# Kernel tuning notes

Measured on AMD Instinct MI355X. Metric: run time of the kernel, lower is better.

## Reference

```python
import jax, jax.numpy as jnp
import numpy as np

K = 16          # max neighbors per ball query
RADIUS = 1.0    # ball radius
SEQ_LEN = 4
N_POINTS = 8192


def ball_query_idx(xyz, radius, k):
    """PointNet++-style ball query of xyz against itself.
    xyz: [N, 3]. Returns [N, k] int32: the first k in-radius source indices
    (in ascending index order, matching the CUDA kernel's scan order),
    padded with the first in-radius index when fewer than k are found.
    Self-distance is 0 < radius so every row has at least one hit.
    """
    n = xyz.shape[0]
    # squared pairwise distances via the matmul expansion: ||a-b||^2 = ||a||^2 + ||b||^2 - 2 a.b
    sq = jnp.sum(xyz * xyz, axis=-1)                          # [N]
    d2 = sq[:, None] + sq[None, :] - 2.0 * (xyz @ xyz.T)      # [N, N]
    cand = jnp.where(d2 < radius * radius, jnp.arange(n, dtype=jnp.int32)[None, :], n)
    firstk = jnp.sort(cand, axis=-1)[:, :k]                   # first k hits in index order, n = no-hit sentinel
    first = firstk[:, :1]                                     # first in-radius index (always valid)
    return jnp.where(firstk == n, first, firstk)              # pad missing slots with first hit


def setup_inputs() -> dict:
    key = jax.random.key(0)
    k1, k2 = jax.random.split(key)
    pc_source = jax.random.normal(k1, (1, N_POINTS, 3), dtype=jnp.float32)
    pred_flow = jax.random.normal(k2, (SEQ_LEN, N_POINTS, 3), dtype=jnp.float32)
    return {"pc_source": pc_source, "pred_flow": pred_flow}


def reference(pc_source, pred_flow):
    # idx from pc_source (batch 1), broadcast across the sequence (idx.repeat in torch)
    idx = ball_query_idx(pc_source[0], RADIUS, K)             # [N, k]
    flow = jnp.transpose(pred_flow, (0, 2, 1))                # [S, 3, N]
    nn_flow = flow[:, :, idx]                                 # grouping_operation -> [S, 3, N, k]
    diff = flow[..., None] - nn_flow                          # [S, 3, N, k]
    # p=2 norm over the channel dim (safe sqrt: self-neighbor diff is exactly 0)
    dist = jnp.sqrt(jnp.maximum(jnp.sum(diff * diff, axis=1), 1e-24))  # [S, N, k]
    # .mean(dim=-1) over k, then .mean(dim=-1) over N (no weights branch), then .mean() over S
    return dist.mean(axis=-1).mean(axis=-1).mean()
```

## Files before the change

kernel.cpp:

```cpp
#include <hip/hip_runtime.h>
#include <math.h>

#define NP 8192
#define SEQ 4
#define KNN 16
#define R2 1.0f

__global__ __launch_bounds__(256, 8) void ballq_fused(
    const float* __restrict__ xyz,
    const float* __restrict__ pf,
    float* __restrict__ partial)
{
    const int lane = threadIdx.x & 63;
    const int wv   = threadIdx.x >> 6;
    const int i    = (blockIdx.x << 2) + wv;

    const float xi = xyz[3 * i + 0];
    const float yi = xyz[3 * i + 1];
    const float zi = xyz[3 * i + 2];

    int myNbr = -1;
    int cnt   = 0;
    int first = -1;

    for (int base = 0; base < NP; base += 256) {
        unsigned long long masks[4];
#pragma unroll
        for (int u = 0; u < 4; ++u) {
            const int j = base + (u << 6) + lane;
            const float dx = xyz[3 * j + 0] - xi;
            const float dy = xyz[3 * j + 1] - yi;
            const float dz = xyz[3 * j + 2] - zi;
            masks[u] = __ballot(dx * dx + dy * dy + dz * dz < R2);
        }
#pragma unroll
        for (int u = 0; u < 4; ++u) {
            unsigned long long m = masks[u];
            const int sub = base + (u << 6);
            while (m && cnt < KNN) {
                const int b = __builtin_ctzll(m);
                const int j = sub + b;
                if (cnt == 0) first = j;
                if (lane == cnt) myNbr = j;
                ++cnt;
                m &= m - 1;
            }
        }
        if (cnt >= KNN) break;
    }
    if (myNbr < 0) myNbr = first;

    const int k = lane & 15;
    const int s = lane >> 4;
    const int j = __shfl(myNbr, k);
    const size_t oi = ((size_t)s * NP + i) * 3;
    const size_t oj = ((size_t)s * NP + j) * 3;
    const float dx = pf[oi + 0] - pf[oj + 0];
    const float dy = pf[oi + 1] - pf[oj + 1];
    const float dz = pf[oi + 2] - pf[oj + 2];
    float d = sqrtf(fmaxf(dx * dx + dy * dy + dz * dz, 1e-24f));

#pragma unroll
    for (int off = 32; off > 0; off >>= 1) d += __shfl_xor(d, off);

    __shared__ float sacc[4];
    if (lane == 0) sacc[wv] = d;
    __syncthreads();
    if (threadIdx.x == 0)
        partial[blockIdx.x] = sacc[0] + sacc[1] + sacc[2] + sacc[3];
}

__global__ __launch_bounds__(256) void ballq_reduce(
    const float* __restrict__ partial, int n, float* __restrict__ out)
{
    float s = 0.0f;
    for (int i = threadIdx.x; i < n; i += 256) s += partial[i];
#pragma unroll
    for (int off = 32; off > 0; off >>= 1) s += __shfl_xor(s, off);
    __shared__ float w[4];
    const int lane = threadIdx.x & 63, wv = threadIdx.x >> 6;
    if (lane == 0) w[wv] = s;
    __syncthreads();
    if (threadIdx.x == 0)
        out[0] = (w[0] + w[1] + w[2] + w[3]) * (1.0f / (float)(SEQ * NP * KNN));
}

extern "C" void kernel_launch(void* const* d_in, const int* in_sizes, int n_in,
                              void* d_out, int out_size, void* d_ws, size_t ws_size,
                              hipStream_t stream) {
    const float* xyz = (const float*)d_in[0];
    const float* pf  = (const float*)d_in[1];
    float* partial   = (float*)d_ws;
    float* out       = (float*)d_out;

    const int nblocks = NP / 4;
    ballq_fused<<<nblocks, 256, 0, stream>>>(xyz, pf, partial);
    ballq_reduce<<<1, 256, 0, stream>>>(partial, nblocks, out);
}
```

Before: 73.49 us.

## Prefetch next candidate tile in registers and replace reduce kernel with atomics

The ball-query scan now software-pipelines its candidate loads: while the current 256-point tile is tested, the next tile's coordinates are loaded into registers, which hides global load latency in the early-exit loop. The separate reduction kernel is removed; each block atomically adds its scaled partial sum into the output, which is zeroed first with a memset. The occupancy hint in launch_bounds is also dropped. The extra registers may lower occupancy, and float atomics make the summation order nondeterministic.

```diff
diff --git a/kernel.cpp b/kernel.cpp
--- a/kernel.cpp
+++ b/kernel.cpp
@@ -5,11 +5,12 @@
 #define SEQ 4
 #define KNN 16
 #define R2 1.0f
+#define SCALE (1.0f / (float)(SEQ * NP * KNN))
 
-__global__ __launch_bounds__(256, 8) void ballq_fused(
+__global__ __launch_bounds__(256) void ballq_fused(
     const float* __restrict__ xyz,
     const float* __restrict__ pf,
-    float* __restrict__ partial)
+    float* __restrict__ out)
 {
     const int lane = threadIdx.x & 63;
     const int wv   = threadIdx.x >> 6;
@@ -23,16 +24,34 @@
     int cnt   = 0;
     int first = -1;
 
+    float cx[4], cy[4], cz[4];
+#pragma unroll
+    for (int u = 0; u < 4; ++u) {
+        const int j = (u << 6) + lane;
+        cx[u] = xyz[3 * j + 0];
+        cy[u] = xyz[3 * j + 1];
+        cz[u] = xyz[3 * j + 2];
+    }
+
     for (int base = 0; base < NP; base += 256) {
+        float nx[4], ny[4], nz[4];
+#pragma unroll
+        for (int u = 0; u < 4; ++u) {
+            const int j = (base + 256 + (u << 6) + lane) & (NP - 1);
+            nx[u] = xyz[3 * j + 0];
+            ny[u] = xyz[3 * j + 1];
+            nz[u] = xyz[3 * j + 2];
+        }
+
         unsigned long long masks[4];
 #pragma unroll
         for (int u = 0; u < 4; ++u) {
-            const int j = base + (u << 6) + lane;
-            const float dx = xyz[3 * j + 0] - xi;
-            const float dy = xyz[3 * j + 1] - yi;
-            const float dz = xyz[3 * j + 2] - zi;
+            const float dx = cx[u] - xi;
+            const float dy = cy[u] - yi;
+            const float dz = cz[u] - zi;
             masks[u] = __ballot(dx * dx + dy * dy + dz * dz < R2);
         }
+
 #pragma unroll
         for (int u = 0; u < 4; ++u) {
             unsigned long long m = masks[u];
@@ -47,6 +66,9 @@
             }
         }
         if (cnt >= KNN) break;
+
+#pragma unroll
+        for (int u = 0; u < 4; ++u) { cx[u] = nx[u]; cy[u] = ny[u]; cz[u] = nz[u]; }
     }
     if (myNbr < 0) myNbr = first;
 
@@ -67,22 +89,7 @@
     if (lane == 0) sacc[wv] = d;
     __syncthreads();
     if (threadIdx.x == 0)
-        partial[blockIdx.x] = sacc[0] + sacc[1] + sacc[2] + sacc[3];
-}
-
-__global__ __launch_bounds__(256) void ballq_reduce(
-    const float* __restrict__ partial, int n, float* __restrict__ out)
-{
-    float s = 0.0f;
-    for (int i = threadIdx.x; i < n; i += 256) s += partial[i];
-#pragma unroll
-    for (int off = 32; off > 0; off >>= 1) s += __shfl_xor(s, off);
-    __shared__ float w[4];
-    const int lane = threadIdx.x & 63, wv = threadIdx.x >> 6;
-    if (lane == 0) w[wv] = s;
-    __syncthreads();
-    if (threadIdx.x == 0)
-        out[0] = (w[0] + w[1] + w[2] + w[3]) * (1.0f / (float)(SEQ * NP * KNN));
+        atomicAdd(out, (sacc[0] + sacc[1] + sacc[2] + sacc[3]) * SCALE);
 }
 
 extern "C" void kernel_launch(void* const* d_in, const int* in_sizes, int n_in,
@@ -90,10 +97,8 @@
                               hipStream_t stream) {
     const float* xyz = (const float*)d_in[0];
     const float* pf  = (const float*)d_in[1];
-    float* partial   = (float*)d_ws;
     float* out       = (float*)d_out;
 
-    const int nblocks = NP / 4;
-    ballq_fused<<<nblocks, 256, 0, stream>>>(xyz, pf, partial);
-    ballq_reduce<<<1, 256, 0, stream>>>(partial, nblocks, out);
+    hipMemsetAsync(out, 0, sizeof(float), stream);
+    ballq_fused<<<NP / 4, 256, 0, stream>>>(xyz, pf, out);
 }
```

After: 88.64 us. 20.6% more time.

## Scan 1024 candidates per wave via per-lane bitmasks and prefix-sum compaction

Applied to the files above, without the earlier changes.

Each lane now loads 16 consecutive points with 12 float4 loads and builds a 16-bit in-radius mask, so one wave tests 1024 candidates per iteration instead of 256. Hits are ranked with a wave prefix sum and written in index order to a shared-memory slot array, replacing the serial ctz loop that ran over ballot masks. This cuts per-iteration overhead and widens loads, but uses many more registers (48 floats), drops the occupancy hint in launch bounds, and may scan more points than needed before the early exit.

```diff
diff --git a/kernel.cpp b/kernel.cpp
--- a/kernel.cpp
+++ b/kernel.cpp
@@ -5,8 +5,12 @@
 #define SEQ 4
 #define KNN 16
 #define R2 1.0f
+#define NBLK (NP / 4)
+#define WSZ 1024
+#define CPL 16
+#define SCALE (1.0f / (float)(SEQ * NP * KNN))
 
-__global__ __launch_bounds__(256, 8) void ballq_fused(
+__global__ __launch_bounds__(256) void ballq_main(
     const float* __restrict__ xyz,
     const float* __restrict__ pf,
     float* __restrict__ partial)
@@ -19,36 +23,55 @@
     const float yi = xyz[3 * i + 1];
     const float zi = xyz[3 * i + 2];
 
+    __shared__ int slots[4][KNN];
+
     int myNbr = -1;
     int cnt   = 0;
-    int first = -1;
 
-    for (int base = 0; base < NP; base += 256) {
-        unsigned long long masks[4];
+    for (int base = 0; base < NP; base += WSZ) {
+        float f[48];
+        const float4* p = (const float4*)xyz + ((3 * base) >> 2) + 12 * lane;
 #pragma unroll
-        for (int u = 0; u < 4; ++u) {
-            const int j = base + (u << 6) + lane;
-            const float dx = xyz[3 * j + 0] - xi;
-            const float dy = xyz[3 * j + 1] - yi;
-            const float dz = xyz[3 * j + 2] - zi;
-            masks[u] = __ballot(dx * dx + dy * dy + dz * dz < R2);
+        for (int j = 0; j < 12; ++j) ((float4*)f)[j] = p[j];
+
+        unsigned m = 0;
+#pragma unroll
+        for (int u = 0; u < CPL; ++u) {
+            const float dx = f[3 * u + 0] - xi;
+            const float dy = f[3 * u + 1] - yi;
+            const float dz = f[3 * u + 2] - zi;
+            m |= (unsigned)(dx * dx + dy * dy + dz * dz < R2) << u;
         }
+
+        const int c = __popc(m);
+        int pfx = c;
 #pragma unroll
-        for (int u = 0; u < 4; ++u) {
-            unsigned long long m = masks[u];
-            const int sub = base + (u << 6);
-            while (m && cnt < KNN) {
-                const int b = __builtin_ctzll(m);
-                const int j = sub + b;
-                if (cnt == 0) first = j;
-                if (lane == cnt) myNbr = j;
-                ++cnt;
-                m &= m - 1;
-            }
+        for (int off = 1; off < 64; off <<= 1) {
+            const int t = __shfl_up(pfx, off);
+            if (lane >= off) pfx += t;
         }
+        const int excl  = pfx - c;
+        const int total = __shfl(pfx, 63);
+
+        unsigned mm = m;
+        int r = 0;
+        while (mm) {
+            const int rank = cnt + excl + r;
+            if (rank >= KNN) break;
+            const int b = __builtin_ctz(mm);
+            slots[wv][rank] = base + CPL * lane + b;
+            mm &= mm - 1;
+            ++r;
+        }
+
+        const int newcnt = cnt + total;
+        if (lane >= cnt && lane < KNN && lane < newcnt)
+            myNbr = slots[wv][lane];
+        cnt = newcnt;
         if (cnt >= KNN) break;
     }
-    if (myNbr < 0) myNbr = first;
+    const int firstHit = __shfl(myNbr, 0);
+    if (myNbr < 0) myNbr = firstHit;
 
     const int k = lane & 15;
     const int s = lane >> 4;
@@ -71,10 +94,10 @@
 }
 
 __global__ __launch_bounds__(256) void ballq_reduce(
-    const float* __restrict__ partial, int n, float* __restrict__ out)
+    const float* __restrict__ partial, float* __restrict__ out)
 {
     float s = 0.0f;
-    for (int i = threadIdx.x; i < n; i += 256) s += partial[i];
+    for (int t = threadIdx.x; t < NBLK; t += 256) s += partial[t];
 #pragma unroll
     for (int off = 32; off > 0; off >>= 1) s += __shfl_xor(s, off);
     __shared__ float w[4];
@@ -82,7 +105,7 @@
     if (lane == 0) w[wv] = s;
     __syncthreads();
     if (threadIdx.x == 0)
-        out[0] = (w[0] + w[1] + w[2] + w[3]) * (1.0f / (float)(SEQ * NP * KNN));
+        out[0] = (w[0] + w[1] + w[2] + w[3]) * SCALE;
 }
 
 extern "C" void kernel_launch(void* const* d_in, const int* in_sizes, int n_in,
@@ -93,7 +116,6 @@
     float* partial   = (float*)d_ws;
     float* out       = (float*)d_out;
 
-    const int nblocks = NP / 4;
-    ballq_fused<<<nblocks, 256, 0, stream>>>(xyz, pf, partial);
-    ballq_reduce<<<1, 256, 0, stream>>>(partial, nblocks, out);
+    ballq_main<<<NBLK, 256, 0, stream>>>(xyz, pf, partial);
+    ballq_reduce<<<1, 256, 0, stream>>>(partial, out);
 }
```

Result: slower. 78.17 us (+6.4%).

## Replace serial ballot-bit scan with mbcnt ranking into shared slots, widen batch

Applied to the files above, without the earlier changes.

Each wave's serial while-loop, which pulled hits out of the ballot mask one bit at a time, is replaced by a parallel per-lane rank from mbcnt. Hit lanes write their index straight into a shared-memory slot array, with padding falling back to slot 0. The scan batch grows from 256 to 1024 candidates per iteration with all loads issued first, to expose more memory parallelism. The 8-waves-per-SIMD occupancy hint is dropped, the 16-entry register arrays raise register use, and a larger batch can overscan past the point where 16 hits are already found. The reduce kernel is also hard-wired to 2048 partials read as float4.

```diff
diff --git a/kernel.cpp b/kernel.cpp
--- a/kernel.cpp
+++ b/kernel.cpp
@@ -5,8 +5,10 @@
 #define SEQ 4
 #define KNN 16
 #define R2 1.0f
+#define NBLK (NP / 4)
+#define SCALE (1.0f / (float)(SEQ * NP * KNN))
 
-__global__ __launch_bounds__(256, 8) void ballq_fused(
+__global__ __launch_bounds__(256) void ballq_main(
     const float* __restrict__ xyz,
     const float* __restrict__ pf,
     float* __restrict__ partial)
@@ -19,40 +21,42 @@
     const float yi = xyz[3 * i + 1];
     const float zi = xyz[3 * i + 2];
 
-    int myNbr = -1;
-    int cnt   = 0;
-    int first = -1;
+    __shared__ int slots[4][KNN];
+    int cnt = 0;
 
-    for (int base = 0; base < NP; base += 256) {
-        unsigned long long masks[4];
+    for (int base = 0; base < NP; base += 1024) {
+        float fx[16], fy[16], fz[16];
 #pragma unroll
-        for (int u = 0; u < 4; ++u) {
+        for (int u = 0; u < 16; ++u) {
             const int j = base + (u << 6) + lane;
-            const float dx = xyz[3 * j + 0] - xi;
-            const float dy = xyz[3 * j + 1] - yi;
-            const float dz = xyz[3 * j + 2] - zi;
-            masks[u] = __ballot(dx * dx + dy * dy + dz * dz < R2);
+            fx[u] = xyz[3 * j + 0];
+            fy[u] = xyz[3 * j + 1];
+            fz[u] = xyz[3 * j + 2];
         }
 #pragma unroll
-        for (int u = 0; u < 4; ++u) {
-            unsigned long long m = masks[u];
-            const int sub = base + (u << 6);
-            while (m && cnt < KNN) {
-                const int b = __builtin_ctzll(m);
-                const int j = sub + b;
-                if (cnt == 0) first = j;
-                if (lane == cnt) myNbr = j;
-                ++cnt;
-                m &= m - 1;
+        for (int u = 0; u < 16; ++u) {
+            const float dx = fx[u] - xi;
+            const float dy = fy[u] - yi;
+            const float dz = fz[u] - zi;
+            const bool hit = dx * dx + dy * dy + dz * dz < R2;
+            const unsigned long long m = __ballot(hit);
+            if (hit) {
+                const int rank = __builtin_amdgcn_mbcnt_hi(
+                    (unsigned)(m >> 32),
+                    __builtin_amdgcn_mbcnt_lo((unsigned)m, 0));
+                const int g = cnt + rank;
+                if (g < KNN) slots[wv][g] = base + (u << 6) + lane;
             }
+            cnt += __popcll(m);
         }
         if (cnt >= KNN) break;
     }
-    if (myNbr < 0) myNbr = first;
 
-    const int k = lane & 15;
+    int si = lane & 15;
+    if (si >= cnt) si = 0;
+    const int j = slots[wv][si];
+
     const int s = lane >> 4;
-    const int j = __shfl(myNbr, k);
     const size_t oi = ((size_t)s * NP + i) * 3;
     const size_t oj = ((size_t)s * NP + j) * 3;
     const float dx = pf[oi + 0] - pf[oj + 0];
@@ -71,10 +75,12 @@
 }
 
 __global__ __launch_bounds__(256) void ballq_reduce(
-    const float* __restrict__ partial, int n, float* __restrict__ out)
+    const float* __restrict__ partial, float* __restrict__ out)
 {
-    float s = 0.0f;
-    for (int i = threadIdx.x; i < n; i += 256) s += partial[i];
+    const float4* p4 = (const float4*)partial;
+    const float4 a = p4[threadIdx.x];
+    const float4 b = p4[threadIdx.x + 256];
+    float s = (a.x + a.y + a.z + a.w) + (b.x + b.y + b.z + b.w);
 #pragma unroll
     for (int off = 32; off > 0; off >>= 1) s += __shfl_xor(s, off);
     __shared__ float w[4];
@@ -82,7 +88,7 @@
     if (lane == 0) w[wv] = s;
     __syncthreads();
     if (threadIdx.x == 0)
-        out[0] = (w[0] + w[1] + w[2] + w[3]) * (1.0f / (float)(SEQ * NP * KNN));
+        out[0] = (w[0] + w[1] + w[2] + w[3]) * SCALE;
 }
 
 extern "C" void kernel_launch(void* const* d_in, const int* in_sizes, int n_in,
@@ -93,7 +99,6 @@
     float* partial   = (float*)d_ws;
     float* out       = (float*)d_out;
 
-    const int nblocks = NP / 4;
-    ballq_fused<<<nblocks, 256, 0, stream>>>(xyz, pf, partial);
-    ballq_reduce<<<1, 256, 0, stream>>>(partial, nblocks, out);
+    ballq_main<<<NBLK, 256, 0, stream>>>(xyz, pf, partial);
+    ballq_reduce<<<1, 256, 0, stream>>>(partial, out);
 }
```

Measured after the change: 69.71 us. 1.05x faster.
